# Optimization experiments

Hardware: AMD Instinct MI355X
Metric: run time of the kernel (lower is better)

Reference implementation:

```python
import jax, jax.numpy as jnp
import numpy as np

B, T, D = 2, 2048, 1024
H, K = 16, 64  # num_heads, key_size (value_size == key_size)


def setup_inputs() -> dict:
    key = jax.random.key(0)
    ks = jax.random.split(key, 9)
    # xavier-uniform-ish scale for square-ish projections
    def xavier(k, shape):
        fan_in, fan_out = shape[0], shape[1]
        lim = jnp.sqrt(6.0 / (fan_in + fan_out))
        return jax.random.uniform(k, shape, jnp.float32, -lim, lim)
    return {
        "x_q": jax.random.normal(ks[0], (B, T, D), jnp.float32),
        "Wq": xavier(ks[1], (D, H * K)),
        "bq": jnp.zeros((H * K,), jnp.float32),
        "Wk": xavier(ks[2], (D, H * K)),
        "bk": jnp.zeros((H * K,), jnp.float32),
        "Wv": xavier(ks[3], (D, H * K)),
        "bv": jnp.zeros((H * K,), jnp.float32),
        "Wo": xavier(ks[4], (H * K, D)),
        "bo": jnp.zeros((D,), jnp.float32),
    }


def reference(x_q, Wq, bq, Wk, bk, Wv, bv, Wo, bo):
    # self-attention: x_k = x_v = x_q
    q = (x_q @ Wq + bq).reshape(B, T, H, K)
    k = (x_q @ Wk + bk).reshape(B, T, H, K)
    v = (x_q @ Wv + bv).reshape(B, T, H, K)
    # dense_dot_product_attention, mask=None
    logits = jnp.einsum('bqhd,bkhd->bhqk', q, k) / jnp.sqrt(jnp.asarray(K, k.dtype))
    attn_w = jax.nn.softmax(logits, axis=-1)  # [B,H,Tq,Tk]
    attn = jnp.einsum('bhqk,bkhd->bqhd', attn_w, v).reshape(B, T, H * K)
    out = attn @ Wo + bo  # [B,T,D]
    return out
```

## Files before the change

### kernel.cpp

```cpp
#include <hip/hip_runtime.h>
#include <hip/hip_bf16.h>
#include <stdint.h>

#define B_  2
#define T_  2048
#define D_  1024
#define H_  16
#define KS  64
#define M_  (B_*T_)

typedef unsigned short u16;
typedef __bf16 bf16x8 __attribute__((ext_vector_type(8)));
typedef __bf16 bf16x4 __attribute__((ext_vector_type(4)));
typedef float  f32x4  __attribute__((ext_vector_type(4)));

#define AS1 __attribute__((address_space(1)))
#define AS3 __attribute__((address_space(3)))

__device__ inline u16 f2bf(float x){
  union { float f; uint32_t u; } v; v.f = x;
  uint32_t r = (v.u + 0x7fffu + ((v.u >> 16) & 1u)) >> 16;
  return (u16)r;
}

__device__ inline void gl_lds16(const u16* g, u16* l){
  __builtin_amdgcn_global_load_lds((AS1 void*)(const_cast<u16*>(g)),
                                   (AS3 void*)l, 16, 0, 0);
}

__global__ __launch_bounds__(256) void k_cvt_x(const float* __restrict__ x,
                                               u16* __restrict__ xb){
  int i = blockIdx.x * 256 + threadIdx.x;
  float4 v = ((const float4*)x)[i];
  ushort4 o;
  o.x = f2bf(v.x); o.y = f2bf(v.y); o.z = f2bf(v.z); o.w = f2bf(v.w);
  ((ushort4*)xb)[i] = o;
}

__global__ __launch_bounds__(256) void k_tconv_w(const float* __restrict__ W0,
                                                 const float* __restrict__ W1,
                                                 const float* __restrict__ W2,
                                                 const float* __restrict__ W3,
                                                 u16* __restrict__ out){
  const float* W = (blockIdx.z==0)?W0:(blockIdx.z==1)?W1:(blockIdx.z==2)?W2:W3;
  u16* o = out + (size_t)blockIdx.z * 1024 * 1024;
  __shared__ float tile[32][33];
  int tx = threadIdx.x, ty = threadIdx.y;
  int kb = blockIdx.y * 32, nb = blockIdx.x * 32;
  for(int i=0;i<4;i++) tile[ty+8*i][tx] = W[(size_t)(kb+ty+8*i)*1024 + nb+tx];
  __syncthreads();
  for(int i=0;i<4;i++){
    int n = nb + ty + 8*i;
    o[(size_t)n*1024 + kb + tx] = f2bf(tile[tx][ty+8*i]);
  }
}

__global__ __launch_bounds__(256) void k_gemm_qkv(const u16* __restrict__ xb,
                                                  const u16* __restrict__ wt,
                                                  const float* __restrict__ bq,
                                                  const float* __restrict__ bk,
                                                  const float* __restrict__ bv,
                                                  u16* __restrict__ qkv,
                                                  u16* __restrict__ vt){
  int widx = blockIdx.x >> 3;
  int n0   = (blockIdx.x & 7) * 128;
  int m0   = blockIdx.y * 128;
  const u16* BT = wt + (size_t)widx * (1024*1024);
  const float* bias = (widx==0)?bq:(widx==1)?bk:bv;
  u16* out = qkv + (size_t)widx * (4*1024*1024);
  float oscale = (widx==0) ? 0.125f * 1.44269504088896f : 1.0f;

  __shared__ u16 Asm[128*64];
  __shared__ u16 Bsm[128*64];
  int t = threadIdx.x;
  int lane = t & 63, w = t >> 6, wm = w >> 1, wn = w & 1;
  int l15 = lane & 15, l4 = lane >> 4;
  f32x4 zero = {0.f,0.f,0.f,0.f};
  f32x4 acc[4][4];
  for(int i=0;i<4;i++) for(int j=0;j<4;j++) acc[i][j] = zero;
  int srow = t >> 3, schunk = t & 7;

  for(int kt=0; kt<16; ++kt){
    __syncthreads();
    int kb = kt * 64;
    for(int i=0;i<4;i++){
      int row = i*32 + srow;
      int gch = schunk ^ (row & 7);
      gl_lds16(xb + (size_t)(m0+row)*1024 + kb + gch*8, Asm + row*64 + schunk*8);
      gl_lds16(BT + (size_t)(n0+row)*1024 + kb + gch*8, Bsm + row*64 + schunk*8);
    }
    __syncthreads();
    for(int c=0;c<2;c++){
      bf16x8 af[4], bfr[4];
      for(int mt=0;mt<4;mt++){
        int row = wm*64 + mt*16 + l15;
        int idx = (row*64 + c*32 + l4*8) ^ ((row & 7) << 3);
        af[mt] = *(const bf16x8*)(Asm + idx);
      }
      for(int nt=0;nt<4;nt++){
        int row = wn*64 + nt*16 + l15;
        int idx = (row*64 + c*32 + l4*8) ^ ((row & 7) << 3);
        bfr[nt] = *(const bf16x8*)(Bsm + idx);
      }
      for(int mt=0;mt<4;mt++)
        for(int nt=0;nt<4;nt++)
          acc[mt][nt] = __builtin_amdgcn_mfma_f32_16x16x32_bf16(af[mt], bfr[nt], acc[mt][nt], 0,0,0);
    }
  }
  if(widx == 2){
    for(int nt=0;nt<4;nt++){
      int nbase = n0 + wn*64 + nt*16 + l15;
      float bv_ = bias[nbase];
      int h = nbase >> 6, kk = nbase & 63;
      for(int mt=0;mt<4;mt++){
        int m = m0 + wm*64 + mt*16 + l4*4;
        int b = m >> 11, tt = m & 2047;
        bf16x4 pk;
        for(int r=0;r<4;r++) pk[r] = (__bf16)(acc[mt][nt][r] + bv_);
        *(bf16x4*)(vt + (((size_t)(b*H_ + h)*64 + kk)*T_) + tt) = pk;
      }
    }
  } else {
    for(int nt=0;nt<4;nt++){
      int nbase = n0 + wn*64 + nt*16 + l15;
      float bv_ = bias[nbase];
      int h = nbase >> 6, kk = nbase & 63;
      for(int mt=0;mt<4;mt++){
        for(int r=0;r<4;r++){
          int m = m0 + wm*64 + mt*16 + l4*4 + r;
          int b = m >> 11, tt = m & 2047;
          out[(((size_t)(b*H_ + h)*T_ + tt) << 6) + kk] = f2bf((acc[mt][nt][r] + bv_) * oscale);
        }
      }
    }
  }
}

__global__ __launch_bounds__(256) void k_attn(const u16* __restrict__ Q,
                                              const u16* __restrict__ Kg,
                                              const u16* __restrict__ VT,
                                              u16* __restrict__ attn_out){
  int bx = blockIdx.x;
  int qt = bx & 31, h = (bx >> 5) & 15, b = bx >> 9;
  int bh = b*H_ + h;
  const u16* Qh = Q  + (size_t)bh * T_ * 64;
  const u16* Kh = Kg + (size_t)bh * T_ * 64;
  const u16* Vh = VT + (size_t)bh * 64 * T_;
  __shared__ u16 Ksm[2][64*64];
  __shared__ u16 Vsm[2][64*64];
  __shared__ u16 Psm[4][16*64];
  int t = threadIdx.x, lane = t & 63, w = t >> 6;
  int l15 = lane & 15, l4 = lane >> 4;

  bf16x8 qf[2];
  int qrow = qt*64 + w*16 + l15;
  for(int c=0;c<2;c++)
    qf[c] = *(const bf16x8*)(Qh + (size_t)qrow*64 + c*32 + l4*8);

  bf16x8 ones;
  for(int j=0;j<8;j++) ones[j] = (__bf16)1.0f;

  f32x4 zero = {0.f,0.f,0.f,0.f};
  f32x4 accT[4];
  for(int g=0;g<4;g++) accT[g] = zero;
  f32x4 accL = zero;
  float m_r = -3.0e38f;

  int srow = t >> 3, schunk = t & 7;

  for(int i=0;i<2;i++){
    int row = i*32 + srow;
    int gch = schunk ^ (row & 7);
    gl_lds16(Kh + (size_t)row*64 + gch*8,  &Ksm[0][row*64 + schunk*8]);
    gl_lds16(Vh + (size_t)row*T_ + gch*8,  &Vsm[0][row*64 + schunk*8]);
  }
  __syncthreads();

  int cur = 0;
  for(int tile=0; tile<32; ++tile){
    if(tile+1 < 32){
      int kvb = (tile+1)*64;
      for(int i=0;i<2;i++){
        int row = i*32 + srow;
        int gch = schunk ^ (row & 7);
        gl_lds16(Kh + (size_t)(kvb+row)*64 + gch*8, &Ksm[cur^1][row*64 + schunk*8]);
        gl_lds16(Vh + (size_t)row*T_ + kvb + gch*8, &Vsm[cur^1][row*64 + schunk*8]);
      }
    }

    f32x4 s[4];
    for(int g=0;g<4;g++) s[g] = zero;
    __builtin_amdgcn_s_setprio(1);
    for(int c=0;c<2;c++){
      for(int g=0;g<4;g++){
        int row = g*16 + l15;
        int idx = (row*64 + c*32 + l4*8) ^ ((row & 7) << 3);
        bf16x8 kf = *(const bf16x8*)(&Ksm[cur][idx]);
        s[g] = __builtin_amdgcn_mfma_f32_16x16x32_bf16(kf, qf[c], s[g], 0,0,0);
      }
    }
    __builtin_amdgcn_s_setprio(0);

    float t0 = fmaxf(fmaxf(fmaxf(s[0][0], s[0][1]), s[0][2]), s[0][3]);
    float t1 = fmaxf(fmaxf(fmaxf(s[1][0], s[1][1]), s[1][2]), s[1][3]);
    float t2 = fmaxf(fmaxf(fmaxf(s[2][0], s[2][1]), s[2][2]), s[2][3]);
    float t3 = fmaxf(fmaxf(fmaxf(s[3][0], s[3][1]), s[3][2]), s[3][3]);
    float pmax = fmaxf(fmaxf(fmaxf(t0, t1), t2), t3);
    pmax = fmaxf(pmax, __shfl_xor(pmax, 16));
    pmax = fmaxf(pmax, __shfl_xor(pmax, 32));
    if(__any(pmax > m_r + 8.f)){
      float mnew  = fmaxf(m_r, pmax);
      float alpha = __builtin_amdgcn_exp2f(m_r - mnew);
      m_r = mnew;
      for(int g=0;g<4;g++){
        f32x4 a = accT[g];
        for(int r=0;r<4;r++) a[r] *= alpha;
        accT[g] = a;
      }
      for(int r=0;r<4;r++) accL[r] *= alpha;
    }
    for(int g=0;g<4;g++)
      for(int r=0;r<4;r++)
        s[g][r] = __builtin_amdgcn_exp2f(s[g][r] - m_r);

    for(int g=0;g<4;g++){
      bf16x4 pk;
      for(int r=0;r<4;r++) pk[r] = (__bf16)s[g][r];
      int idx = (l15*64 + g*16 + l4*4) ^ ((l15 & 7) << 3);
      *(bf16x4*)(&Psm[w][idx]) = pk;
    }

    __builtin_amdgcn_s_setprio(1);
    for(int c=0;c<2;c++){
      int idx_p = (l15*64 + c*32 + l4*8) ^ ((l15 & 7) << 3);
      bf16x8 pf = *(const bf16x8*)(&Psm[w][idx_p]);
      accL = __builtin_amdgcn_mfma_f32_16x16x32_bf16(ones, pf, accL, 0,0,0);
      for(int g=0;g<4;g++){
        int row = g*16 + l15;
        int idx = (row*64 + c*32 + l4*8) ^ ((row & 7) << 3);
        bf16x8 vf = *(const bf16x8*)(&Vsm[cur][idx]);
        accT[g] = __builtin_amdgcn_mfma_f32_16x16x32_bf16(vf, pf, accT[g], 0,0,0);
      }
    }
    __builtin_amdgcn_s_setprio(0);

    __syncthreads();
    cur ^= 1;
  }

  float oinv = 1.0f / accL[0];
  int m = b*T_ + qt*64 + w*16 + l15;
  for(int g=0;g<4;g++){
    bf16x4 pk;
    for(int r=0;r<4;r++) pk[r] = (__bf16)(accT[g][r] * oinv);
    *(bf16x4*)(attn_out + (size_t)m*1024 + h*64 + g*16 + l4*4) = pk;
  }
}

__global__ __launch_bounds__(256) void k_gemm_out(const u16* __restrict__ A,
                                                  const u16* __restrict__ BT,
                                                  const float* __restrict__ bias,
                                                  float* __restrict__ out){
  int n0 = blockIdx.x * 128;
  int m0 = blockIdx.y * 64;
  __shared__ u16 Asm[64*64];
  __shared__ u16 Bsm[128*64];
  int t = threadIdx.x;
  int lane = t & 63, w = t >> 6, wm = w >> 1, wn = w & 1;
  int l15 = lane & 15, l4 = lane >> 4;
  f32x4 zero = {0.f,0.f,0.f,0.f};
  f32x4 acc[2][4];
  for(int i=0;i<2;i++) for(int j=0;j<4;j++) acc[i][j] = zero;
  int srow = t >> 3, schunk = t & 7;

  for(int kt=0; kt<16; ++kt){
    __syncthreads();
    int kb = kt * 64;
    for(int i=0;i<2;i++){
      int row = i*32 + srow;
      int gch = schunk ^ (row & 7);
      gl_lds16(A  + (size_t)(m0+row)*1024 + kb + gch*8, Asm + row*64 + schunk*8);
    }
    for(int i=0;i<4;i++){
      int row = i*32 + srow;
      int gch = schunk ^ (row & 7);
      gl_lds16(BT + (size_t)(n0+row)*1024 + kb + gch*8, Bsm + row*64 + schunk*8);
    }
    __syncthreads();
    for(int c=0;c<2;c++){
      bf16x8 af[2], bfr[4];
      for(int mt=0;mt<2;mt++){
        int row = wm*32 + mt*16 + l15;
        int idx = (row*64 + c*32 + l4*8) ^ ((row & 7) << 3);
        af[mt] = *(const bf16x8*)(Asm + idx);
      }
      for(int nt=0;nt<4;nt++){
        int row = wn*64 + nt*16 + l15;
        int idx = (row*64 + c*32 + l4*8) ^ ((row & 7) << 3);
        bfr[nt] = *(const bf16x8*)(Bsm + idx);
      }
      for(int mt=0;mt<2;mt++)
        for(int nt=0;nt<4;nt++)
          acc[mt][nt] = __builtin_amdgcn_mfma_f32_16x16x32_bf16(af[mt], bfr[nt], acc[mt][nt], 0,0,0);
    }
  }
  for(int nt=0;nt<4;nt++){
    int nbase = n0 + wn*64 + nt*16 + l15;
    float bv_ = bias[nbase];
    for(int mt=0;mt<2;mt++){
      for(int r=0;r<4;r++){
        int m = m0 + wm*32 + mt*16 + l4*4 + r;
        out[(size_t)m*1024 + nbase] = acc[mt][nt][r] + bv_;
      }
    }
  }
}

extern "C" void kernel_launch(void* const* d_in, const int* in_sizes, int n_in,
                              void* d_out, int out_size, void* d_ws, size_t ws_size,
                              hipStream_t stream){
  const float* x  = (const float*)d_in[0];
  const float* Wq = (const float*)d_in[1];
  const float* bq = (const float*)d_in[2];
  const float* Wk = (const float*)d_in[3];
  const float* bk = (const float*)d_in[4];
  const float* Wv = (const float*)d_in[5];
  const float* bv = (const float*)d_in[6];
  const float* Wo = (const float*)d_in[7];
  const float* bo = (const float*)d_in[8];
  float* out = (float*)d_out;
  char* ws = (char*)d_ws;

  u16* xb  = (u16*)(ws);
  u16* wt  = (u16*)(ws + (8u  << 20));
  u16* qkv = (u16*)(ws + (16u << 20));
  u16* vt  = (u16*)(ws + (40u << 20));
  u16* at  = (u16*)(ws + (48u << 20));

  k_cvt_x   <<<4096, 256, 0, stream>>>(x, xb);
  k_tconv_w <<<dim3(32,32,4), dim3(32,8), 0, stream>>>(Wq, Wk, Wv, Wo, wt);
  k_gemm_qkv<<<dim3(24,32), 256, 0, stream>>>(xb, wt, bq, bk, bv, qkv, vt);
  k_attn    <<<1024, 256, 0, stream>>>(qkv, qkv + (size_t)4*1024*1024, vt, at);
  k_gemm_out<<<dim3(8,64), 256, 0, stream>>>(at, wt + (size_t)3*1024*1024, bo, out);
}
```

Measured before the change: 212.8 us.

## Transpose MFMA operands for vectorized epilogue stores and unroll attention double-buffer loop

The Q/K projection and output GEMMs swap the MFMA A/B operands so each lane holds four consecutive output columns, which lets the epilogues do float4 bias loads and 8- or 16-byte vector stores instead of scalar scattered stores. The attention kernel unrolls its tile loop by two so the double-buffer index is a compile-time constant, hoists the swizzle computation, and adds a minimum-occupancy hint of 3 to launch bounds. This targets uncoalesced global writes and address arithmetic, at the cost of more code and possible register pressure under the occupancy hint.

```diff
diff --git a/kernel.cpp b/kernel.cpp
--- a/kernel.cpp
+++ b/kernel.cpp
@@ -102,9 +102,15 @@
         int idx = (row*64 + c*32 + l4*8) ^ ((row & 7) << 3);
         bfr[nt] = *(const bf16x8*)(Bsm + idx);
       }
-      for(int mt=0;mt<4;mt++)
-        for(int nt=0;nt<4;nt++)
-          acc[mt][nt] = __builtin_amdgcn_mfma_f32_16x16x32_bf16(af[mt], bfr[nt], acc[mt][nt], 0,0,0);
+      if(widx < 2){
+        for(int mt=0;mt<4;mt++)
+          for(int nt=0;nt<4;nt++)
+            acc[mt][nt] = __builtin_amdgcn_mfma_f32_16x16x32_bf16(bfr[nt], af[mt], acc[mt][nt], 0,0,0);
+      } else {
+        for(int mt=0;mt<4;mt++)
+          for(int nt=0;nt<4;nt++)
+            acc[mt][nt] = __builtin_amdgcn_mfma_f32_16x16x32_bf16(af[mt], bfr[nt], acc[mt][nt], 0,0,0);
+      }
     }
   }
   if(widx == 2){
@@ -122,24 +128,27 @@
     }
   } else {
     for(int nt=0;nt<4;nt++){
-      int nbase = n0 + wn*64 + nt*16 + l15;
-      float bv_ = bias[nbase];
-      int h = nbase >> 6, kk = nbase & 63;
+      int nb = n0 + wn*64 + nt*16 + l4*4;
+      float4 b4 = *(const float4*)&bias[nb];
+      int h = nb >> 6, kk = nb & 63;
       for(int mt=0;mt<4;mt++){
-        for(int r=0;r<4;r++){
-          int m = m0 + wm*64 + mt*16 + l4*4 + r;
-          int b = m >> 11, tt = m & 2047;
-          out[(((size_t)(b*H_ + h)*T_ + tt) << 6) + kk] = f2bf((acc[mt][nt][r] + bv_) * oscale);
-        }
-      }
-    }
-  }
-}
-
-__global__ __launch_bounds__(256) void k_attn(const u16* __restrict__ Q,
-                                              const u16* __restrict__ Kg,
-                                              const u16* __restrict__ VT,
-                                              u16* __restrict__ attn_out){
+        int m = m0 + wm*64 + mt*16 + l15;
+        int b = m >> 11, tt = m & 2047;
+        bf16x4 pk;
+        pk[0] = (__bf16)((acc[mt][nt][0] + b4.x) * oscale);
+        pk[1] = (__bf16)((acc[mt][nt][1] + b4.y) * oscale);
+        pk[2] = (__bf16)((acc[mt][nt][2] + b4.z) * oscale);
+        pk[3] = (__bf16)((acc[mt][nt][3] + b4.w) * oscale);
+        *(bf16x4*)(out + (((size_t)(b*H_ + h)*T_ + tt) << 6) + kk) = pk;
+      }
+    }
+  }
+}
+
+__global__ __launch_bounds__(256, 3) void k_attn(const u16* __restrict__ Q,
+                                                 const u16* __restrict__ Kg,
+                                                 const u16* __restrict__ VT,
+                                                 u16* __restrict__ attn_out){
   int bx = blockIdx.x;
   int qt = bx & 31, h = (bx >> 5) & 15, b = bx >> 9;
   int bh = b*H_ + h;
@@ -167,25 +176,21 @@
   float m_r = -3.0e38f;
 
   int srow = t >> 3, schunk = t & 7;
-
-  for(int i=0;i<2;i++){
-    int row = i*32 + srow;
-    int gch = schunk ^ (row & 7);
-    gl_lds16(Kh + (size_t)row*64 + gch*8,  &Ksm[0][row*64 + schunk*8]);
-    gl_lds16(Vh + (size_t)row*T_ + gch*8,  &Vsm[0][row*64 + schunk*8]);
-  }
+  int gchS = schunk ^ (srow & 7);
+
+  gl_lds16(Kh + (size_t)srow*64      + gchS*8, &Ksm[0][srow*64      + schunk*8]);
+  gl_lds16(Kh + (size_t)(srow+32)*64 + gchS*8, &Ksm[0][(srow+32)*64 + schunk*8]);
+  gl_lds16(Vh + (size_t)srow*T_      + gchS*8, &Vsm[0][srow*64      + schunk*8]);
+  gl_lds16(Vh + (size_t)(srow+32)*T_ + gchS*8, &Vsm[0][(srow+32)*64 + schunk*8]);
   __syncthreads();
 
-  int cur = 0;
-  for(int tile=0; tile<32; ++tile){
+  auto body = [&](int tile, int cur){
     if(tile+1 < 32){
       int kvb = (tile+1)*64;
-      for(int i=0;i<2;i++){
-        int row = i*32 + srow;
-        int gch = schunk ^ (row & 7);
-        gl_lds16(Kh + (size_t)(kvb+row)*64 + gch*8, &Ksm[cur^1][row*64 + schunk*8]);
-        gl_lds16(Vh + (size_t)row*T_ + kvb + gch*8, &Vsm[cur^1][row*64 + schunk*8]);
-      }
+      gl_lds16(Kh + (size_t)(kvb+srow)*64    + gchS*8, &Ksm[cur^1][srow*64      + schunk*8]);
+      gl_lds16(Kh + (size_t)(kvb+srow+32)*64 + gchS*8, &Ksm[cur^1][(srow+32)*64 + schunk*8]);
+      gl_lds16(Vh + (size_t)srow*T_      + kvb + gchS*8, &Vsm[cur^1][srow*64      + schunk*8]);
+      gl_lds16(Vh + (size_t)(srow+32)*T_ + kvb + gchS*8, &Vsm[cur^1][(srow+32)*64 + schunk*8]);
     }
 
     f32x4 s[4];
@@ -245,7 +250,11 @@
     __builtin_amdgcn_s_setprio(0);
 
     __syncthreads();
-    cur ^= 1;
+  };
+
+  for(int t2=0; t2<16; ++t2){
+    body(2*t2,   0);
+    body(2*t2+1, 1);
   }
 
   float oinv = 1.0f / accL[0];
@@ -301,17 +310,20 @@
       }
       for(int mt=0;mt<2;mt++)
         for(int nt=0;nt<4;nt++)
-          acc[mt][nt] = __builtin_amdgcn_mfma_f32_16x16x32_bf16(af[mt], bfr[nt], acc[mt][nt], 0,0,0);
+          acc[mt][nt] = __builtin_amdgcn_mfma_f32_16x16x32_bf16(bfr[nt], af[mt], acc[mt][nt], 0,0,0);
     }
   }
   for(int nt=0;nt<4;nt++){
-    int nbase = n0 + wn*64 + nt*16 + l15;
-    float bv_ = bias[nbase];
+    int nb = n0 + wn*64 + nt*16 + l4*4;
+    float4 b4 = *(const float4*)&bias[nb];
     for(int mt=0;mt<2;mt++){
-      for(int r=0;r<4;r++){
-        int m = m0 + wm*32 + mt*16 + l4*4 + r;
-        out[(size_t)m*1024 + nbase] = acc[mt][nt][r] + bv_;
-      }
+      int m = m0 + wm*32 + mt*16 + l15;
+      float4 o;
+      o.x = acc[mt][nt][0] + b4.x;
+      o.y = acc[mt][nt][1] + b4.y;
+      o.z = acc[mt][nt][2] + b4.z;
+      o.w = acc[mt][nt][3] + b4.w;
+      *(float4*)&out[(size_t)m*1024 + nb] = o;
     }
   }
 }
```

After: 222.3 us. 4.5% more time.
